# Kernel tuning notes

Measured on AMD Instinct MI355X. Metric: run time of the kernel, lower is better.

Reference implementation:

```python
import jax, jax.numpy as jnp
import numpy as np

DIM = 768
NUM_HEADS = 12
HEAD_DIM = DIM // NUM_HEADS
SCALE = HEAD_DIM ** -0.5
EPS = 1e-6


def setup_inputs() -> dict:
    key = jax.random.key(0)
    k_x, k_p, k_qkv, k_proj = jax.random.split(key, 4)
    B, N = 16, 577
    x = jax.random.normal(k_x, (B, N, DIM), dtype=jnp.float32)
    # binary keep/drop policy per token (as produced by an upstream gumbel gate)
    policy = jax.random.randint(k_p, (B, N, 1), 0, 2).astype(jnp.float32)
    Wqkv = jax.random.normal(k_qkv, (DIM, 3 * DIM), dtype=jnp.float32) * 0.02
    bqkv = jnp.zeros((3 * DIM,), dtype=jnp.float32)
    Wproj = jax.random.normal(k_proj, (DIM, DIM), dtype=jnp.float32) * 0.02
    bproj = jnp.zeros((DIM,), dtype=jnp.float32)
    return {"x": x, "policy": policy, "Wqkv": Wqkv, "bqkv": bqkv,
            "Wproj": Wproj, "bproj": bproj}


def reference(x, policy, Wqkv, bqkv, Wproj, bproj):
    B, N, C = x.shape
    # qkv projection -> [3, B, H, N, Dh]
    qkv = (x @ Wqkv + bqkv).reshape(B, N, 3, NUM_HEADS, HEAD_DIM)
    qkv = jnp.transpose(qkv, (2, 0, 3, 1, 4))
    q, k, v = qkv[0], qkv[1], qkv[2]
    # scaled attention logits [B, H, N, N]
    attn = jnp.einsum("bhnd,bhmd->bhnm", q, k) * SCALE
    # policy-masked softmax (training-mode formula: eye keeps self-attention alive)
    ap = policy.reshape(B, 1, 1, N)
    eye = jnp.eye(N, dtype=ap.dtype).reshape(1, 1, N, N)
    ap = ap + (1.0 - ap) * eye
    max_att = jnp.max(attn, axis=-1, keepdims=True)
    e = jnp.exp(attn - max_att) * ap
    attn = (e + EPS / N) / (jnp.sum(e, axis=-1, keepdims=True) + EPS)
    # attend and project
    out = jnp.einsum("bhnm,bhmd->bhnd", attn, v)
    out = jnp.transpose(out, (0, 2, 1, 3)).reshape(B, N, C)
    return out @ Wproj + bproj
```

## Files before the change

### kernel.cpp

```cpp
#include <hip/hip_runtime.h>
#include <hip/hip_bf16.h>

#define QKVC   2304
#define NHEAD  12
#define NTOK   577
#define NBATCH 16
#define NROWS  (NBATCH * NTOK)
#define NPAD   640
#define SCALE  0.125f
#define EPSV   1e-6f

typedef __bf16  bf16x8 __attribute__((ext_vector_type(8)));
typedef float   f32x4  __attribute__((ext_vector_type(4)));

__device__ __forceinline__ unsigned short f2bf(float f) {
    union { float f; unsigned u; } v; v.f = f;
    unsigned r = v.u + 0x7FFFu + ((v.u >> 16) & 1u);
    return (unsigned short)(r >> 16);
}
__device__ __forceinline__ unsigned short f2bf_trunc(float f) {
    return (unsigned short)(__float_as_uint(f) >> 16);
}
__device__ __forceinline__ f32x4 mfma16(bf16x8 a, bf16x8 b, f32x4 c) {
    return __builtin_amdgcn_mfma_f32_16x16x32_bf16(a, b, c, 0, 0, 0);
}

#define GLDS16(g, l) __builtin_amdgcn_global_load_lds( \
    (const __attribute__((address_space(1))) unsigned int*)(g), \
    (__attribute__((address_space(3))) unsigned int*)(l), 16, 0, 0)

__global__ void k_convert_x(const float* __restrict__ x, unsigned short* __restrict__ xb) {
    int idx = blockIdx.x * 256 + threadIdx.x;
    float4 v = ((const float4*)x)[idx];
    ushort4 o;
    o.x = f2bf(v.x); o.y = f2bf(v.y); o.z = f2bf(v.z); o.w = f2bf(v.w);
    ((ushort4*)xb)[idx] = o;
}

__global__ void k_transpose_w(const float* __restrict__ src, unsigned short* __restrict__ dst,
                              int K, int N) {
    __shared__ unsigned short lt[64 * 72];
    int t  = threadIdx.x;
    int n0 = blockIdx.x * 64, k0 = blockIdx.y * 64;
    int kk = t >> 4, nn = (t & 15) * 4;
    for (int i = 0; i < 4; i++) {
        int kr = kk + i * 16;
        float4 v = *(const float4*)&src[(size_t)(k0 + kr) * N + n0 + nn];
        lt[(nn + 0) * 72 + kr] = f2bf(v.x);
        lt[(nn + 1) * 72 + kr] = f2bf(v.y);
        lt[(nn + 2) * 72 + kr] = f2bf(v.z);
        lt[(nn + 3) * 72 + kr] = f2bf(v.w);
    }
    __syncthreads();
    int n = t >> 2, seg = (t & 3) * 16;
    uint4 a = *(uint4*)&lt[n * 72 + seg];
    uint4 b = *(uint4*)&lt[n * 72 + seg + 8];
    *(uint4*)&dst[(size_t)(n0 + n) * K + k0 + seg]     = a;
    *(uint4*)&dst[(size_t)(n0 + n) * K + k0 + seg + 8] = b;
}

template <bool F32OUT>
__global__ __launch_bounds__(256, 3)
void k_gemm(const unsigned short* __restrict__ A, const unsigned short* __restrict__ B,
            const float* __restrict__ bias, void* __restrict__ outp, int Ncols) {
    __shared__ unsigned short SL[24576];
    unsigned short (*As)[4096] = (unsigned short (*)[4096])SL;
    unsigned short (*Bs)[4096] = (unsigned short (*)[4096])&SL[12288];
    int t = threadIdx.x;
    int lane = t & 63, wave = t >> 6, quad = lane >> 4, l15 = lane & 15;
    int wm = wave >> 1, wn = wave & 1;
    int nT = Ncols >> 7;
    int mLocal = blockIdx.x & 7;
    int rest = blockIdx.x >> 3;
    int n0 = (rest % nT) * 128;
    int m0 = ((rest / nT) * 8 + mLocal) * 128;

    const unsigned short* ga0 = A + (size_t)(m0 + wave * 32 + (lane >> 2)) * 768 + (lane & 3) * 8;
    const unsigned short* ga1 = ga0 + (size_t)16 * 768;
    const unsigned short* gb0 = B + (size_t)(n0 + wave * 32 + (lane >> 2)) * 768 + (lane & 3) * 8;
    const unsigned short* gb1 = gb0 + (size_t)16 * 768;
    unsigned lo = wave * 1024;

    f32x4 acc[4][4] = {};

    GLDS16(ga0,      &As[0][lo]); GLDS16(ga1,      &As[0][lo + 512]);
    GLDS16(gb0,      &Bs[0][lo]); GLDS16(gb1,      &Bs[0][lo + 512]);
    GLDS16(ga0 + 32, &As[1][lo]); GLDS16(ga1 + 32, &As[1][lo + 512]);
    GLDS16(gb0 + 32, &Bs[1][lo]); GLDS16(gb1 + 32, &Bs[1][lo + 512]);

    #pragma unroll 3
    for (int kt = 0; kt < 24; kt++) {
        int buf = kt % 3;
        if (kt == 23) { asm volatile("s_waitcnt vmcnt(0)" ::: "memory"); }
        else          { asm volatile("s_waitcnt vmcnt(4)" ::: "memory"); }
        asm volatile("s_barrier" ::: "memory");
        if (kt < 22) {
            int nb = buf + 2; if (nb >= 3) nb -= 3;
            int ko = (kt + 2) * 32;
            GLDS16(ga0 + ko, &As[nb][lo]); GLDS16(ga1 + ko, &As[nb][lo + 512]);
            GLDS16(gb0 + ko, &Bs[nb][lo]); GLDS16(gb1 + ko, &Bs[nb][lo + 512]);
        }
        bf16x8 af[4], bfr[4];
        for (int i = 0; i < 4; i++) {
            af[i]  = *(const bf16x8*)&As[buf][(wm * 64 + i * 16 + l15) * 32 + quad * 8];
            bfr[i] = *(const bf16x8*)&Bs[buf][(wn * 64 + i * 16 + l15) * 32 + quad * 8];
        }
        for (int mi = 0; mi < 4; mi++)
            for (int ni = 0; ni < 4; ni++)
                acc[mi][ni] = mfma16(af[mi], bfr[ni], acc[mi][ni]);
    }
    asm volatile("" ::: "memory");

    if constexpr (F32OUT) {
        for (int ni = 0; ni < 4; ni++) {
            int col = n0 + wn * 64 + ni * 16 + l15;
            float bv = bias[col];
            for (int mi = 0; mi < 4; mi++) {
                int rowm = m0 + wm * 64 + mi * 16 + quad * 4;
                for (int r = 0; r < 4; r++) {
                    int m = rowm + r;
                    if (m < NROWS)
                        ((float*)outp)[(size_t)m * Ncols + col] = acc[mi][ni][r] + bv;
                }
            }
        }
    } else {
        __syncthreads();
        for (int ni = 0; ni < 4; ni++) {
            int colL = wn * 64 + ni * 16 + l15;
            float bv = bias[n0 + colL];
            for (int mi = 0; mi < 4; mi++) {
                int rowL = wm * 64 + mi * 16 + quad * 4;
                for (int r = 0; r < 4; r++)
                    SL[(rowL + r) * 132 + colL] = f2bf(acc[mi][ni][r] + bv);
            }
        }
        __syncthreads();
        for (int rr = 0; rr < 8; rr++) {
            int row = rr * 16 + (t >> 4);
            int m = m0 + row;
            if (m < NROWS) {
                uint4 v = *(uint4*)&SL[row * 132 + (t & 15) * 8];
                *(uint4*)&((unsigned short*)outp)[(size_t)m * Ncols + n0 + (t & 15) * 8] = v;
            }
        }
    }
}

__global__ void k_vtrans(const unsigned short* __restrict__ qkv, unsigned short* __restrict__ vt) {
    __shared__ unsigned short lt[64 * 72];
    int t = threadIdx.x;
    int b = blockIdx.z, h = blockIdx.y, tt = blockIdx.x;
    for (int i = t; i < 512; i += 256) {
        int row = i >> 3, seg = (i & 7) * 8;
        int tok = tt * 64 + row;
        uint4 v = {0, 0, 0, 0};
        if (tok < NTOK)
            v = *(const uint4*)&qkv[(size_t)(b * NTOK + tok) * QKVC + 1536 + h * 64 + seg];
        *(uint4*)&lt[row * 72 + seg] = v;
    }
    __syncthreads();
    for (int i = t; i < 512; i += 256) {
        int d = i >> 3, ts = i & 7;
        unsigned short tmp[8];
        for (int j = 0; j < 8; j++) tmp[j] = lt[(ts * 8 + j) * 72 + d];
        *(uint4*)&vt[((size_t)((b * NHEAD + h) * 64) + d) * NPAD + tt * 64 + ts * 8] =
            *(uint4*)tmp;
    }
}

__global__ __launch_bounds__(256, 4)
void k_attn(const unsigned short* __restrict__ qkv, const unsigned short* __restrict__ vt,
            const float* __restrict__ policy, unsigned short* __restrict__ ao) {
    __shared__ unsigned short Ks[64 * 72];
    __shared__ unsigned short Vs[64 * 72];
    __shared__ unsigned short Ps[4][32 * 72];
    __shared__ float pol[NPAD];
    int t = threadIdx.x;
    int lane = t & 63, wave = t >> 6, quad = lane >> 4, l15 = lane & 15;
    int b = blockIdx.z, h = blockIdx.y, qt = blockIdx.x;
    const unsigned short* qbase = qkv + (size_t)(b * NTOK) * QKVC + h * 64;
    const unsigned short* kbase = qkv + (size_t)(b * NTOK) * QKVC + 768 + h * 64;
    const unsigned short* vbase = vt + (size_t)(b * NHEAD + h) * 64 * NPAD;

    for (int i = t; i < NPAD; i += 256)
        pol[i] = (i < NTOK) ? policy[b * NTOK + i] : 0.f;

    bf16x8 qf[2][2];
    for (int mi = 0; mi < 2; mi++) {
        const unsigned short* qp =
            qbase + (size_t)(qt * 128 + mi * 64 + wave * 16 + l15) * QKVC + quad * 8;
        qf[mi][0] = *(const bf16x8*)qp;
        qf[mi][1] = *(const bf16x8*)(qp + 32);
    }
    bf16x8 onesf;
    for (int j = 0; j < 8; j++) onesf[j] = (__bf16)1.0f;
    f32x4 o[2][4] = {};
    f32x4 ls[2] = {};
    int rowtok0[2];
    for (int mi = 0; mi < 2; mi++)
        rowtok0[mi] = qt * 128 + mi * 64 + wave * 16 + quad * 4;
    __syncthreads();

    for (int kt = 0; kt < 10; kt++) {
        int key0 = kt * 64;
        for (int i = t; i < 512; i += 256) {
            int row = i >> 3, seg = (i & 7) * 8;
            *(uint4*)&Ks[row * 72 + seg] = *(const uint4*)&kbase[(size_t)(key0 + row) * QKVC + seg];
            *(uint4*)&Vs[row * 72 + seg] = *(const uint4*)&vbase[(size_t)row * NPAD + key0 + seg];
        }
        __syncthreads();

        for (int ci = 0; ci < 4; ci++) {
            bf16x8 kf0 = *(const bf16x8*)&Ks[(ci * 16 + l15) * 72 + quad * 8];
            bf16x8 kf1 = *(const bf16x8*)&Ks[(ci * 16 + l15) * 72 + 32 + quad * 8];
            int col = key0 + ci * 16 + l15;
            float pc = pol[col];
            for (int mi = 0; mi < 2; mi++) {
                f32x4 a = {};
                a = mfma16(qf[mi][0], kf0, a);
                a = mfma16(qf[mi][1], kf1, a);
                for (int r = 0; r < 4; r++) {
                    float ap = (col == rowtok0[mi] + r) ? 1.f : pc;
                    float e = __expf(a[r] * SCALE) * ap;
                    Ps[wave][(mi * 16 + quad * 4 + r) * 72 + ci * 16 + l15] = f2bf_trunc(e);
                }
            }
        }
        __asm__ volatile("s_waitcnt lgkmcnt(0)" ::: "memory");
        bf16x8 pf[2][2];
        for (int mi = 0; mi < 2; mi++) {
            pf[mi][0] = *(const bf16x8*)&Ps[wave][(mi * 16 + l15) * 72 + quad * 8];
            pf[mi][1] = *(const bf16x8*)&Ps[wave][(mi * 16 + l15) * 72 + 32 + quad * 8];
            ls[mi] = mfma16(pf[mi][0], onesf, ls[mi]);
            ls[mi] = mfma16(pf[mi][1], onesf, ls[mi]);
        }
        for (int di = 0; di < 4; di++) {
            bf16x8 vf0 = *(const bf16x8*)&Vs[(di * 16 + l15) * 72 + quad * 8];
            bf16x8 vf1 = *(const bf16x8*)&Vs[(di * 16 + l15) * 72 + 32 + quad * 8];
            for (int mi = 0; mi < 2; mi++) {
                o[mi][di] = mfma16(pf[mi][0], vf0, o[mi][di]);
                o[mi][di] = mfma16(pf[mi][1], vf1, o[mi][di]);
            }
        }
        __syncthreads();
    }

    for (int mi = 0; mi < 2; mi++) {
        for (int r = 0; r < 4; r++) {
            int tok = rowtok0[mi] + r;
            if (tok < NTOK) {
                float inv = __builtin_amdgcn_rcpf(ls[mi][r] + EPSV);
                for (int di = 0; di < 4; di++) {
                    float val = o[mi][di][r] * inv;
                    ao[((size_t)(b * NTOK + tok)) * 768 + h * 64 + di * 16 + l15] = f2bf(val);
                }
            }
        }
    }
}

extern "C" void kernel_launch(void* const* d_in, const int* in_sizes, int n_in,
                              void* d_out, int out_size, void* d_ws, size_t ws_size,
                              hipStream_t stream) {
    const float* x      = (const float*)d_in[0];
    const float* policy = (const float*)d_in[1];
    const float* Wqkv   = (const float*)d_in[2];
    const float* bqkv   = (const float*)d_in[3];
    const float* Wproj  = (const float*)d_in[4];
    const float* bproj  = (const float*)d_in[5];
    float* out = (float*)d_out;

    unsigned short* p = (unsigned short*)d_ws;
    unsigned short* xb     = p;
    unsigned short* ao     = p; p += (size_t)NROWS * 768;
    unsigned short* wqkvt  = p; p += (size_t)QKVC * 768;
    unsigned short* wprojt = p; p += (size_t)768 * 768;
    unsigned short* qkvb   = p; p += (size_t)NROWS * QKVC;
    unsigned short* vt     = p; p += (size_t)NBATCH * NHEAD * 64 * NPAD;

    int mT = (NROWS + 127) / 128;
    int mG = (mT + 7) / 8;

    k_convert_x<<<(NROWS * 768 / 4) / 256, 256, 0, stream>>>(x, xb);
    k_transpose_w<<<dim3(QKVC / 64, 768 / 64), 256, 0, stream>>>(Wqkv, wqkvt, 768, QKVC);
    k_transpose_w<<<dim3(768 / 64, 768 / 64), 256, 0, stream>>>(Wproj, wprojt, 768, 768);
    k_gemm<false><<<mG * 8 * (QKVC / 128), 256, 0, stream>>>(
        xb, wqkvt, bqkv, (void*)qkvb, QKVC);
    k_vtrans<<<dim3(NPAD / 64, NHEAD, NBATCH), 256, 0, stream>>>(qkvb, vt);
    k_attn<<<dim3(NPAD / 128, NHEAD, NBATCH), 256, 0, stream>>>(qkvb, vt, policy, ao);
    k_gemm<true><<<mG * 8 * (768 / 128), 256, 0, stream>>>(
        ao, wprojt, bproj, (void*)out, 768);
}
```

Baseline: 216.1 us.

## Register-staged double-buffered GEMM with padded LDS; fuse prep kernels into one launch

The GEMM drops direct global-to-LDS loads over a triple buffer. Tiles are now prefetched into registers two k-steps ahead and written to a double-buffered LDS tile whose row stride is padded to avoid bank conflicts on the MFMA fragment reads. The x conversion and both weight transposes are merged into one kernel launch to cut launch overhead. The register staging adds VGPR pressure and extra LDS store instructions, which could hurt occupancy at launch bounds of 3 blocks per CU.

```diff
diff --git a/kernel.cpp b/kernel.cpp
--- a/kernel.cpp
+++ b/kernel.cpp
@@ -9,6 +9,7 @@
 #define NPAD   640
 #define SCALE  0.125f
 #define EPSV   1e-6f
+#define LSTR   36
 
 typedef __bf16  bf16x8 __attribute__((ext_vector_type(8)));
 typedef float   f32x4  __attribute__((ext_vector_type(4)));
@@ -25,23 +26,10 @@
     return __builtin_amdgcn_mfma_f32_16x16x32_bf16(a, b, c, 0, 0, 0);
 }
 
-#define GLDS16(g, l) __builtin_amdgcn_global_load_lds( \
-    (const __attribute__((address_space(1))) unsigned int*)(g), \
-    (__attribute__((address_space(3))) unsigned int*)(l), 16, 0, 0)
-
-__global__ void k_convert_x(const float* __restrict__ x, unsigned short* __restrict__ xb) {
-    int idx = blockIdx.x * 256 + threadIdx.x;
-    float4 v = ((const float4*)x)[idx];
-    ushort4 o;
-    o.x = f2bf(v.x); o.y = f2bf(v.y); o.z = f2bf(v.z); o.w = f2bf(v.w);
-    ((ushort4*)xb)[idx] = o;
-}
-
-__global__ void k_transpose_w(const float* __restrict__ src, unsigned short* __restrict__ dst,
-                              int K, int N) {
+__device__ void transpose_tile(const float* __restrict__ src, unsigned short* __restrict__ dst,
+                               int K, int N, int bx, int by, int t) {
     __shared__ unsigned short lt[64 * 72];
-    int t  = threadIdx.x;
-    int n0 = blockIdx.x * 64, k0 = blockIdx.y * 64;
+    int n0 = bx * 64, k0 = by * 64;
     int kk = t >> 4, nn = (t & 15) * 4;
     for (int i = 0; i < 4; i++) {
         int kr = kk + i * 16;
@@ -59,13 +47,31 @@
     *(uint4*)&dst[(size_t)(n0 + n) * K + k0 + seg + 8] = b;
 }
 
+#define NCONV (NROWS * 768 / 4 / 256)
+__global__ void k_prep(const float* __restrict__ x, unsigned short* __restrict__ xb,
+                       const float* __restrict__ Wqkv, unsigned short* __restrict__ wqkvt,
+                       const float* __restrict__ Wproj, unsigned short* __restrict__ wprojt) {
+    int id = blockIdx.x, t = threadIdx.x;
+    if (id < NCONV) {
+        int idx = id * 256 + t;
+        float4 v = ((const float4*)x)[idx];
+        ushort4 o;
+        o.x = f2bf(v.x); o.y = f2bf(v.y); o.z = f2bf(v.z); o.w = f2bf(v.w);
+        ((ushort4*)xb)[idx] = o;
+    } else if (id < NCONV + 432) {
+        int i2 = id - NCONV;
+        transpose_tile(Wqkv, wqkvt, 768, QKVC, i2 % 36, i2 / 36, t);
+    } else {
+        int i2 = id - NCONV - 432;
+        transpose_tile(Wproj, wprojt, 768, 768, i2 % 12, i2 / 12, t);
+    }
+}
+
 template <bool F32OUT>
 __global__ __launch_bounds__(256, 3)
 void k_gemm(const unsigned short* __restrict__ A, const unsigned short* __restrict__ B,
             const float* __restrict__ bias, void* __restrict__ outp, int Ncols) {
-    __shared__ unsigned short SL[24576];
-    unsigned short (*As)[4096] = (unsigned short (*)[4096])SL;
-    unsigned short (*Bs)[4096] = (unsigned short (*)[4096])&SL[12288];
+    __shared__ unsigned short SL[2][2][128 * LSTR];
     int t = threadIdx.x;
     int lane = t & 63, wave = t >> 6, quad = lane >> 4, l15 = lane & 15;
     int wm = wave >> 1, wn = wave & 1;
@@ -75,41 +81,50 @@
     int n0 = (rest % nT) * 128;
     int m0 = ((rest / nT) * 8 + mLocal) * 128;
 
-    const unsigned short* ga0 = A + (size_t)(m0 + wave * 32 + (lane >> 2)) * 768 + (lane & 3) * 8;
-    const unsigned short* ga1 = ga0 + (size_t)16 * 768;
-    const unsigned short* gb0 = B + (size_t)(n0 + wave * 32 + (lane >> 2)) * 768 + (lane & 3) * 8;
-    const unsigned short* gb1 = gb0 + (size_t)16 * 768;
-    unsigned lo = wave * 1024;
+    int srow = wave * 32 + (lane >> 2);
+    int schk = (lane & 3) * 8;
+    const unsigned short* gA = A + (size_t)(m0 + srow) * 768 + schk;
+    const unsigned short* gB = B + (size_t)(n0 + srow) * 768 + schk;
+    int w0 = srow * LSTR + schk, w1 = (srow + 16) * LSTR + schk;
 
     f32x4 acc[4][4] = {};
-
-    GLDS16(ga0,      &As[0][lo]); GLDS16(ga1,      &As[0][lo + 512]);
-    GLDS16(gb0,      &Bs[0][lo]); GLDS16(gb1,      &Bs[0][lo + 512]);
-    GLDS16(ga0 + 32, &As[1][lo]); GLDS16(ga1 + 32, &As[1][lo + 512]);
-    GLDS16(gb0 + 32, &Bs[1][lo]); GLDS16(gb1 + 32, &Bs[1][lo + 512]);
-
-    #pragma unroll 3
-    for (int kt = 0; kt < 24; kt++) {
-        int buf = kt % 3;
-        if (kt == 23) { asm volatile("s_waitcnt vmcnt(0)" ::: "memory"); }
-        else          { asm volatile("s_waitcnt vmcnt(4)" ::: "memory"); }
+    uint4 s0[4], s1[4];
+    s0[0] = *(const uint4*)(gA);      s0[1] = *(const uint4*)(gA + 16 * 768);
+    s0[2] = *(const uint4*)(gB);      s0[3] = *(const uint4*)(gB + 16 * 768);
+    s1[0] = *(const uint4*)(gA + 32); s1[1] = *(const uint4*)(gA + 16 * 768 + 32);
+    s1[2] = *(const uint4*)(gB + 32); s1[3] = *(const uint4*)(gB + 16 * 768 + 32);
+    *(uint4*)&SL[0][0][w0] = s0[0];   *(uint4*)&SL[0][0][w1] = s0[1];
+    *(uint4*)&SL[0][1][w0] = s0[2];   *(uint4*)&SL[0][1][w1] = s0[3];
+
+    auto body = [&](int kt, uint4* sc, uint4* sw) {
+        asm volatile("s_waitcnt lgkmcnt(0)" ::: "memory");
         asm volatile("s_barrier" ::: "memory");
+        int buf = kt & 1;
         if (kt < 22) {
-            int nb = buf + 2; if (nb >= 3) nb -= 3;
             int ko = (kt + 2) * 32;
-            GLDS16(ga0 + ko, &As[nb][lo]); GLDS16(ga1 + ko, &As[nb][lo + 512]);
-            GLDS16(gb0 + ko, &Bs[nb][lo]); GLDS16(gb1 + ko, &Bs[nb][lo + 512]);
+            sc[0] = *(const uint4*)(gA + ko); sc[1] = *(const uint4*)(gA + 16 * 768 + ko);
+            sc[2] = *(const uint4*)(gB + ko); sc[3] = *(const uint4*)(gB + 16 * 768 + ko);
         }
         bf16x8 af[4], bfr[4];
         for (int i = 0; i < 4; i++) {
-            af[i]  = *(const bf16x8*)&As[buf][(wm * 64 + i * 16 + l15) * 32 + quad * 8];
-            bfr[i] = *(const bf16x8*)&Bs[buf][(wn * 64 + i * 16 + l15) * 32 + quad * 8];
+            af[i]  = *(const bf16x8*)&SL[buf][0][(wm * 64 + i * 16 + l15) * LSTR + quad * 8];
+            bfr[i] = *(const bf16x8*)&SL[buf][1][(wn * 64 + i * 16 + l15) * LSTR + quad * 8];
         }
         for (int mi = 0; mi < 4; mi++)
             for (int ni = 0; ni < 4; ni++)
                 acc[mi][ni] = mfma16(af[mi], bfr[ni], acc[mi][ni]);
-    }
-    asm volatile("" ::: "memory");
+        if (kt < 23) {
+            if (kt >= 22) asm volatile("s_waitcnt vmcnt(0)" ::: "memory");
+            else          asm volatile("s_waitcnt vmcnt(4)" ::: "memory");
+            int nb = buf ^ 1;
+            *(uint4*)&SL[nb][0][w0] = sw[0]; *(uint4*)&SL[nb][0][w1] = sw[1];
+            *(uint4*)&SL[nb][1][w0] = sw[2]; *(uint4*)&SL[nb][1][w1] = sw[3];
+        }
+    };
+    for (int k2 = 0; k2 < 12; k2++) {
+        body(2 * k2,     s0, s1);
+        body(2 * k2 + 1, s1, s0);
+    }
 
     if constexpr (F32OUT) {
         for (int ni = 0; ni < 4; ni++) {
@@ -125,6 +140,7 @@
             }
         }
     } else {
+        unsigned short* RP = (unsigned short*)SL;
         __syncthreads();
         for (int ni = 0; ni < 4; ni++) {
             int colL = wn * 64 + ni * 16 + l15;
@@ -132,7 +148,7 @@
             for (int mi = 0; mi < 4; mi++) {
                 int rowL = wm * 64 + mi * 16 + quad * 4;
                 for (int r = 0; r < 4; r++)
-                    SL[(rowL + r) * 132 + colL] = f2bf(acc[mi][ni][r] + bv);
+                    RP[(rowL + r) * 132 + colL] = f2bf(acc[mi][ni][r] + bv);
             }
         }
         __syncthreads();
@@ -140,7 +156,7 @@
             int row = rr * 16 + (t >> 4);
             int m = m0 + row;
             if (m < NROWS) {
-                uint4 v = *(uint4*)&SL[row * 132 + (t & 15) * 8];
+                uint4 v = *(uint4*)&RP[row * 132 + (t & 15) * 8];
                 *(uint4*)&((unsigned short*)outp)[(size_t)m * Ncols + n0 + (t & 15) * 8] = v;
             }
         }
@@ -282,9 +298,7 @@
     int mT = (NROWS + 127) / 128;
     int mG = (mT + 7) / 8;
 
-    k_convert_x<<<(NROWS * 768 / 4) / 256, 256, 0, stream>>>(x, xb);
-    k_transpose_w<<<dim3(QKVC / 64, 768 / 64), 256, 0, stream>>>(Wqkv, wqkvt, 768, QKVC);
-    k_transpose_w<<<dim3(768 / 64, 768 / 64), 256, 0, stream>>>(Wproj, wprojt, 768, 768);
+    k_prep<<<NCONV + 432 + 144, 256, 0, stream>>>(x, xb, Wqkv, wqkvt, Wproj, wprojt);
     k_gemm<false><<<mG * 8 * (QKVC / 128), 256, 0, stream>>>(
         xb, wqkvt, bqkv, (void*)qkvb, QKVC);
     k_vtrans<<<dim3(NPAD / 64, NHEAD, NBATCH), 256, 0, stream>>>(qkvb, vt);
```

Measured after the change: 292.9 us. 35.6% more time.

## Fuse V transpose into QKV GEMM epilogue and merge prep kernels

Applied to the files above, without the earlier changes.

The separate V-transpose kernel is removed. The QKV GEMM epilogue now writes V column tiles straight into the transposed, token-padded vt layout using 2-byte scattered stores from LDS. The x conversion and the two weight transposes are also merged into one launch, selected by block index. This cuts two kernel launches and one round trip of V through global memory, at the cost of narrower stores in the epilogue. The pad tokens of vt are no longer zero-filled, which is a risk if the workspace holds garbage there.

```diff
diff --git a/kernel.cpp b/kernel.cpp
--- a/kernel.cpp
+++ b/kernel.cpp
@@ -29,19 +29,10 @@
     (const __attribute__((address_space(1))) unsigned int*)(g), \
     (__attribute__((address_space(3))) unsigned int*)(l), 16, 0, 0)
 
-__global__ void k_convert_x(const float* __restrict__ x, unsigned short* __restrict__ xb) {
-    int idx = blockIdx.x * 256 + threadIdx.x;
-    float4 v = ((const float4*)x)[idx];
-    ushort4 o;
-    o.x = f2bf(v.x); o.y = f2bf(v.y); o.z = f2bf(v.z); o.w = f2bf(v.w);
-    ((ushort4*)xb)[idx] = o;
-}
-
-__global__ void k_transpose_w(const float* __restrict__ src, unsigned short* __restrict__ dst,
-                              int K, int N) {
+__device__ void transpose_tile(const float* __restrict__ src, unsigned short* __restrict__ dst,
+                               int K, int N, int bx, int by, int t) {
     __shared__ unsigned short lt[64 * 72];
-    int t  = threadIdx.x;
-    int n0 = blockIdx.x * 64, k0 = blockIdx.y * 64;
+    int n0 = bx * 64, k0 = by * 64;
     int kk = t >> 4, nn = (t & 15) * 4;
     for (int i = 0; i < 4; i++) {
         int kr = kk + i * 16;
@@ -59,10 +50,31 @@
     *(uint4*)&dst[(size_t)(n0 + n) * K + k0 + seg + 8] = b;
 }
 
+#define NCONV (NROWS * 768 / 4 / 256)
+__global__ void k_prep(const float* __restrict__ x, unsigned short* __restrict__ xb,
+                       const float* __restrict__ Wqkv, unsigned short* __restrict__ wqkvt,
+                       const float* __restrict__ Wproj, unsigned short* __restrict__ wprojt) {
+    int id = blockIdx.x, t = threadIdx.x;
+    if (id < NCONV) {
+        int idx = id * 256 + t;
+        float4 v = ((const float4*)x)[idx];
+        ushort4 o;
+        o.x = f2bf(v.x); o.y = f2bf(v.y); o.z = f2bf(v.z); o.w = f2bf(v.w);
+        ((ushort4*)xb)[idx] = o;
+    } else if (id < NCONV + 432) {
+        int i2 = id - NCONV;
+        transpose_tile(Wqkv, wqkvt, 768, QKVC, i2 % 36, i2 / 36, t);
+    } else {
+        int i2 = id - NCONV - 432;
+        transpose_tile(Wproj, wprojt, 768, 768, i2 % 12, i2 / 12, t);
+    }
+}
+
 template <bool F32OUT>
 __global__ __launch_bounds__(256, 3)
 void k_gemm(const unsigned short* __restrict__ A, const unsigned short* __restrict__ B,
-            const float* __restrict__ bias, void* __restrict__ outp, int Ncols) {
+            const float* __restrict__ bias, void* __restrict__ outp, int Ncols,
+            unsigned short* __restrict__ vt) {
     __shared__ unsigned short SL[24576];
     unsigned short (*As)[4096] = (unsigned short (*)[4096])SL;
     unsigned short (*Bs)[4096] = (unsigned short (*)[4096])&SL[12288];
@@ -136,36 +148,32 @@
             }
         }
         __syncthreads();
-        for (int rr = 0; rr < 8; rr++) {
-            int row = rr * 16 + (t >> 4);
-            int m = m0 + row;
-            if (m < NROWS) {
-                uint4 v = *(uint4*)&SL[row * 132 + (t & 15) * 8];
-                *(uint4*)&((unsigned short*)outp)[(size_t)m * Ncols + n0 + (t & 15) * 8] = v;
-            }
-        }
-    }
-}
-
-__global__ void k_vtrans(const unsigned short* __restrict__ qkv, unsigned short* __restrict__ vt) {
-    __shared__ unsigned short lt[64 * 72];
-    int t = threadIdx.x;
-    int b = blockIdx.z, h = blockIdx.y, tt = blockIdx.x;
-    for (int i = t; i < 512; i += 256) {
-        int row = i >> 3, seg = (i & 7) * 8;
-        int tok = tt * 64 + row;
-        uint4 v = {0, 0, 0, 0};
-        if (tok < NTOK)
-            v = *(const uint4*)&qkv[(size_t)(b * NTOK + tok) * QKVC + 1536 + h * 64 + seg];
-        *(uint4*)&lt[row * 72 + seg] = v;
-    }
-    __syncthreads();
-    for (int i = t; i < 512; i += 256) {
-        int d = i >> 3, ts = i & 7;
-        unsigned short tmp[8];
-        for (int j = 0; j < 8; j++) tmp[j] = lt[(ts * 8 + j) * 72 + d];
-        *(uint4*)&vt[((size_t)((b * NHEAD + h) * 64) + d) * NPAD + tt * 64 + ts * 8] =
-            *(uint4*)tmp;
+        if (n0 < 1536) {
+            for (int rr = 0; rr < 8; rr++) {
+                int row = rr * 16 + (t >> 4);
+                int m = m0 + row;
+                if (m < NROWS) {
+                    uint4 v = *(uint4*)&SL[row * 132 + (t & 15) * 8];
+                    *(uint4*)&((unsigned short*)outp)[(size_t)m * Ncols + n0 + (t & 15) * 8] = v;
+                }
+            }
+        } else {
+            int h0 = (n0 - 1536) >> 6;
+            for (int i = 0; i < 32; i++) {
+                int c = wave * 32 + i;
+                int h = h0 + (c >> 6), d = c & 63;
+                for (int half = 0; half < 2; half++) {
+                    int lr = half * 64 + lane;
+                    int m = m0 + lr;
+                    if (m < NROWS) {
+                        unsigned bb = (unsigned)m / 577u;
+                        int tok = m - (int)bb * 577;
+                        vt[(((size_t)bb * NHEAD + h) * 64 + d) * NPAD + tok] =
+                            SL[lr * 132 + c];
+                    }
+                }
+            }
+        }
     }
 }
 
@@ -282,13 +290,10 @@
     int mT = (NROWS + 127) / 128;
     int mG = (mT + 7) / 8;
 
-    k_convert_x<<<(NROWS * 768 / 4) / 256, 256, 0, stream>>>(x, xb);
-    k_transpose_w<<<dim3(QKVC / 64, 768 / 64), 256, 0, stream>>>(Wqkv, wqkvt, 768, QKVC);
-    k_transpose_w<<<dim3(768 / 64, 768 / 64), 256, 0, stream>>>(Wproj, wprojt, 768, 768);
+    k_prep<<<NCONV + 432 + 144, 256, 0, stream>>>(x, xb, Wqkv, wqkvt, Wproj, wprojt);
     k_gemm<false><<<mG * 8 * (QKVC / 128), 256, 0, stream>>>(
-        xb, wqkvt, bqkv, (void*)qkvb, QKVC);
-    k_vtrans<<<dim3(NPAD / 64, NHEAD, NBATCH), 256, 0, stream>>>(qkvb, vt);
+        xb, wqkvt, bqkv, (void*)qkvb, QKVC, vt);
     k_attn<<<dim3(NPAD / 128, NHEAD, NBATCH), 256, 0, stream>>>(qkvb, vt, policy, ao);
     k_gemm<true><<<mG * 8 * (768 / 128), 256, 0, stream>>>(
-        ao, wprojt, bproj, (void*)out, 768);
-}
+        ao, wprojt, bproj, (void*)out, 768, nullptr);
+}
```

Measured after the change: 205.1 us. -5.1%, faster.
